# Kernel tuning notes

Measured on AMD Instinct MI355X. Metric: run time of the kernel, lower is better.

The kernel has to match this reference:

```python
import jax, jax.numpy as jnp
import numpy as np

L = 6          # num_layers
B = 2          # batch
F = 16         # num_frames
T = 64         # num_tokens per frame
S = F * T      # seq len = 1024
E = 768        # embed_dim
H = 12         # num_heads
DK = 64        # d_k
DV = 64        # d_v
DFF = 3072     # d_ff
EPS = 1e-5


def setup_inputs() -> dict:
    key = jax.random.key(0)
    ks = jax.random.split(key, 14)
    std = 0.02
    return {
        "x": jax.random.normal(ks[0], (B, S, E), jnp.float32),
        "t_pos": jax.random.normal(ks[1], (1, F, E), jnp.float32) * std,
        "s_pos": jax.random.normal(ks[2], (1, T, E), jnp.float32) * std,
        "Wq": jax.random.normal(ks[3], (L, E, H * DK), jnp.float32) * std,
        "Wk": jax.random.normal(ks[4], (L, E, H * DK), jnp.float32) * std,
        "Wv": jax.random.normal(ks[5], (L, E, H * DV), jnp.float32) * std,
        "Wo": jax.random.normal(ks[6], (L, H * DV, E), jnp.float32) * std,
        "ln1_g": jnp.ones((L, E), jnp.float32),
        "ln1_b": jnp.zeros((L, E), jnp.float32),
        "W1": jax.random.normal(ks[7], (L, E, DFF), jnp.float32) * std,
        "W2": jax.random.normal(ks[8], (L, DFF, E), jnp.float32) * std,
        "ln2_g": jnp.ones((L, E), jnp.float32),
        "ln2_b": jnp.zeros((L, E), jnp.float32),
    }


def _ln(x, g, b):
    m = jnp.mean(x, axis=-1, keepdims=True)
    v = jnp.mean(jnp.square(x - m), axis=-1, keepdims=True)
    return (x - m) * jax.lax.rsqrt(v + EPS) * g + b


def reference(x, t_pos, s_pos, Wq, Wk, Wv, Wo, ln1_g, ln1_b, W1, W2, ln2_g, ln2_b):
    # positional embeddings: frame emb repeated per token, token emb tiled per frame
    t_emb = jnp.repeat(t_pos, T, axis=1)          # [1, S, E]
    s_emb = jnp.tile(s_pos, (1, F, 1))            # [1, S, E]
    x = x + t_emb + s_emb

    # combined causal + pad mask (pad: first embed channel == 0)
    causal = jnp.triu(jnp.ones((S, S), bool), 1)[None, :, :]      # [1, S, S]
    pad = (x[:, :, 0] == 0.0)[:, None, :]                          # [B, 1, S]
    mask = (causal | pad)[:, None, :, :]                           # [B, 1, S, S]

    scale = 1.0 / np.sqrt(DK).astype(np.float32)
    attns = []
    for l in range(L):
        q = (x @ Wq[l]).reshape(B, S, H, DK).transpose(0, 2, 1, 3)  # [B,H,S,DK]
        k = (x @ Wk[l]).reshape(B, S, H, DK).transpose(0, 2, 1, 3)
        v = (x @ Wv[l]).reshape(B, S, H, DV).transpose(0, 2, 1, 3)
        scores = jnp.einsum("bhqd,bhkd->bhqk", q, k) * scale
        scores = jnp.where(mask, -1e9, scores)
        attn = jax.nn.softmax(scores, axis=-1)                      # [B,H,S,S]
        ctx = jnp.einsum("bhqk,bhkd->bhqd", attn, v)
        ctx = ctx.transpose(0, 2, 1, 3).reshape(B, S, H * DV)
        x = _ln(ctx @ Wo[l] + x, ln1_g[l], ln1_b[l])
        h = jax.nn.relu(x @ W1[l]) @ W2[l]
        x = _ln(h + x, ln2_g[l], ln2_b[l])
        attns.append(attn)
    return x, jnp.stack(attns)  # [B,S,E], [L,B,H,S,S]
```

## Files before the change

kernel.cpp:

```cpp
#include <hip/hip_runtime.h>
#include <hip/hip_bf16.h>

#define LYR  6
#define BATCH 2
#define TOK  64
#define SEQ  1024
#define EMB  768
#define HEADS 12
#define HDK  64
#define DFF  3072
#define QKVN 2304

typedef __bf16 bf16_t;
typedef __bf16 bf16x8 __attribute__((ext_vector_type(8)));
typedef float  f32x4  __attribute__((ext_vector_type(4)));
typedef unsigned int u32;

#define GLDS16(g, l) __builtin_amdgcn_global_load_lds( \
    (const __attribute__((address_space(1))) u32*)(g), \
    (__attribute__((address_space(3))) u32*)(l), 16, 0, 0)

static __device__ __forceinline__ unsigned short bfbits(float f) {
    bf16_t b = (bf16_t)f; return *(unsigned short*)&b;
}
static __device__ __forceinline__ float loadf(const void* p, size_t e, int f32) {
    if (f32) return ((const float*)p)[e];
    return (float)((const bf16_t*)p)[e];
}
static __device__ __forceinline__ ushort4 load4bf(const void* p, size_t e, int f32) {
    if (f32) {
        float4 f = *(const float4*)((const float*)p + e);
        ushort4 u; u.x = bfbits(f.x); u.y = bfbits(f.y); u.z = bfbits(f.z); u.w = bfbits(f.w);
        return u;
    }
    return *(const ushort4*)((const unsigned short*)p + e);
}

__global__ __launch_bounds__(256)
void detect_k(const void* w, int* flag)
{
    __shared__ int bad;
    if (threadIdx.x == 0) bad = 0;
    __syncthreads();
    const unsigned short* p = (const unsigned short*)w;
    int local = 0;
    for (int i = threadIdx.x; i < 4096; i += 256) {
        float v = (float)(*(const bf16_t*)&p[i]);
        if (!(v < 1e3f && v > -1e3f)) local = 1;
    }
    if (local) atomicOr(&bad, 1);
    __syncthreads();
    if (threadIdx.x == 0) *flag = bad;
}

__global__ __launch_bounds__(256)
void transp_k(const void* __restrict__ src, bf16_t* __restrict__ dst,
              int K, int N, long sstride, long dstride, long drow0, long dld,
              const int* __restrict__ flagp)
{
    __shared__ unsigned short sm[64][68];
    const int f32 = *flagp;
    const int l  = blockIdx.z;
    const int n0 = blockIdx.x * 64;
    const int k0 = blockIdx.y * 64;
    const int tid = threadIdx.x;
    const int rr = tid >> 4;
    const int cc = tid & 15;

    const size_t sb = (size_t)l * sstride;
#pragma unroll
    for (int p = 0; p < 4; p++) {
        const int kr = rr + p * 16;
        ushort4 u = load4bf(src, sb + (size_t)(k0 + kr) * N + n0 + cc * 4, f32);
        *(ushort4*)&sm[kr][cc * 4] = u;
    }
    __syncthreads();
    const size_t db = (size_t)l * dstride;
#pragma unroll
    for (int p = 0; p < 4; p++) {
        const int r2 = rr + p * 16;
        ushort4 v;
        v.x = sm[cc * 4 + 0][r2];
        v.y = sm[cc * 4 + 1][r2];
        v.z = sm[cc * 4 + 2][r2];
        v.w = sm[cc * 4 + 3][r2];
        *(ushort4*)&dst[db + (size_t)(drow0 + n0 + r2) * dld + k0 + cc * 4] = v;
    }
}

__global__ __launch_bounds__(256)
void vtr_k(const bf16_t* __restrict__ QKV, bf16_t* __restrict__ VT)
{
    __shared__ unsigned short sm[64][68];
    const int z  = blockIdx.y;
    const int s0 = blockIdx.x * 64;
    const int bq = z / HEADS, h = z % HEADS;
    const int tid = threadIdx.x;
    const int rr = tid >> 4, cc = tid & 15;
    const unsigned short* src = (const unsigned short*)QKV
        + (size_t)bq * SEQ * QKVN + 2 * EMB + (size_t)h * HDK;
#pragma unroll
    for (int p = 0; p < 4; p++) {
        const int s = rr + p * 16;
        *(ushort4*)&sm[s][cc * 4] =
            *(const ushort4*)(src + (size_t)(s0 + s) * QKVN + cc * 4);
    }
    __syncthreads();
    unsigned short* dst = (unsigned short*)VT + (size_t)z * HDK * SEQ;
#pragma unroll
    for (int p = 0; p < 4; p++) {
        const int d = rr + p * 16;
        ushort4 v;
        v.x = sm[cc * 4 + 0][d];
        v.y = sm[cc * 4 + 1][d];
        v.z = sm[cc * 4 + 2][d];
        v.w = sm[cc * 4 + 3][d];
        *(ushort4*)(dst + (size_t)d * SEQ + s0 + cc * 4) = v;
    }
}

template<int EPI>
__global__ __launch_bounds__(256)
void gemm64_k(const bf16_t* __restrict__ A, long lda,
              const bf16_t* __restrict__ BT, long ldb,
              void* __restrict__ C, long ldc, int K)
{
    __shared__ __align__(16) unsigned short As[128 * 32];
    __shared__ __align__(16) unsigned short Bs[64 * 32];

    const int tid  = threadIdx.x;
    const int lane = tid & 63;
    const int wave = tid >> 6;
    const int bm = blockIdx.x * 128;
    const int bn = blockIdx.y * 64;
    const int srow = lane >> 2;
    const int scb  = (lane & 3) * 16;
    const int l15 = lane & 15, l4 = lane >> 4;

    const char* gA = (const char*)A;
    const char* gB = (const char*)BT;

    f32x4 acc[2][4];
#pragma unroll
    for (int af = 0; af < 2; af++)
#pragma unroll
        for (int bf = 0; bf < 4; bf++) acc[af][bf] = (f32x4){0.f, 0.f, 0.f, 0.f};

    for (int k0 = 0; k0 < K; k0 += 32) {
#pragma unroll
        for (int j = 0; j < 2; j++) {
            const int rb = (j * 4 + wave) * 16;
            const char* g = gA + ((size_t)(bm + rb + srow) * lda + k0) * 2 + scb;
            GLDS16(g, &As[rb * 32]);
        }
        {
            const int rb = wave * 16;
            const char* g = gB + ((size_t)(bn + rb + srow) * ldb + k0) * 2 + scb;
            GLDS16(g, &Bs[rb * 32]);
        }
        __syncthreads();

        const bf16x8 a0 = *(const bf16x8*)&As[(wave * 32 + l15) * 32 + l4 * 8];
        const bf16x8 a1 = *(const bf16x8*)&As[(wave * 32 + 16 + l15) * 32 + l4 * 8];
#pragma unroll
        for (int bf = 0; bf < 4; bf++) {
            const bf16x8 bv = *(const bf16x8*)&Bs[(bf * 16 + l15) * 32 + l4 * 8];
            acc[0][bf] = __builtin_amdgcn_mfma_f32_16x16x32_bf16(a0, bv, acc[0][bf], 0, 0, 0);
            acc[1][bf] = __builtin_amdgcn_mfma_f32_16x16x32_bf16(a1, bv, acc[1][bf], 0, 0, 0);
        }
        __syncthreads();
    }

#pragma unroll
    for (int af = 0; af < 2; af++) {
#pragma unroll
        for (int bf = 0; bf < 4; bf++) {
#pragma unroll
            for (int r = 0; r < 4; r++) {
                const int row = bm + wave * 32 + af * 16 + l4 * 4 + r;
                const int col = bn + bf * 16 + l15;
                const float v = acc[af][bf][r];
                const size_t idx = (size_t)row * ldc + col;
                if constexpr (EPI == 0) {
                    ((bf16_t*)C)[idx] = (bf16_t)v;
                } else if constexpr (EPI == 1) {
                    ((bf16_t*)C)[idx] = (bf16_t)(v > 0.f ? v : 0.f);
                } else {
                    ((float*)C)[idx] = v;
                }
            }
        }
    }
}

template<int EPI>
__global__ __launch_bounds__(256)
void gemm128_k(const bf16_t* __restrict__ A, long lda,
               const bf16_t* __restrict__ BT, long ldb,
               void* __restrict__ C, long ldc, int K)
{
    __shared__ __align__(16) unsigned short As[128 * 32];
    __shared__ __align__(16) unsigned short Bs[128 * 32];

    const int tid  = threadIdx.x;
    const int lane = tid & 63;
    const int wave = tid >> 6;
    const int bm = blockIdx.x * 128;
    const int bn = blockIdx.y * 128;
    const int srow = lane >> 2;
    const int scb  = (lane & 3) * 16;
    const int l15 = lane & 15, l4 = lane >> 4;
    const int wr = wave >> 1, wc = wave & 1;

    const char* gA = (const char*)A;
    const char* gB = (const char*)BT;

    f32x4 acc[4][4];
#pragma unroll
    for (int m = 0; m < 4; m++)
#pragma unroll
        for (int n = 0; n < 4; n++) acc[m][n] = (f32x4){0.f, 0.f, 0.f, 0.f};

    for (int k0 = 0; k0 < K; k0 += 32) {
#pragma unroll
        for (int j = 0; j < 2; j++) {
            const int rb = (j * 4 + wave) * 16;
            const char* g = gA + ((size_t)(bm + rb + srow) * lda + k0) * 2 + scb;
            GLDS16(g, &As[rb * 32]);
        }
#pragma unroll
        for (int j = 0; j < 2; j++) {
            const int rb = (j * 4 + wave) * 16;
            const char* g = gB + ((size_t)(bn + rb + srow) * ldb + k0) * 2 + scb;
            GLDS16(g, &Bs[rb * 32]);
        }
        __syncthreads();

        bf16x8 a[4], b[4];
#pragma unroll
        for (int m = 0; m < 4; m++)
            a[m] = *(const bf16x8*)&As[(wr * 64 + m * 16 + l15) * 32 + l4 * 8];
#pragma unroll
        for (int n = 0; n < 4; n++)
            b[n] = *(const bf16x8*)&Bs[(wc * 64 + n * 16 + l15) * 32 + l4 * 8];
#pragma unroll
        for (int m = 0; m < 4; m++)
#pragma unroll
            for (int n = 0; n < 4; n++)
                acc[m][n] = __builtin_amdgcn_mfma_f32_16x16x32_bf16(a[m], b[n], acc[m][n], 0, 0, 0);
        __syncthreads();
    }

#pragma unroll
    for (int m = 0; m < 4; m++) {
#pragma unroll
        for (int n = 0; n < 4; n++) {
#pragma unroll
            for (int r = 0; r < 4; r++) {
                const int row = bm + wr * 64 + m * 16 + l4 * 4 + r;
                const int col = bn + wc * 64 + n * 16 + l15;
                const float v = acc[m][n][r];
                const size_t idx = (size_t)row * ldc + col;
                if constexpr (EPI == 0) {
                    ((bf16_t*)C)[idx] = (bf16_t)v;
                } else if constexpr (EPI == 1) {
                    ((bf16_t*)C)[idx] = (bf16_t)(v > 0.f ? v : 0.f);
                } else {
                    ((float*)C)[idx] = v;
                }
            }
        }
    }
}

__global__ __launch_bounds__(256)
void posadd_k(const void* __restrict__ x, const void* __restrict__ tp,
              const void* __restrict__ sp, float* __restrict__ X,
              bf16_t* __restrict__ XB, int* __restrict__ pad,
              const int* __restrict__ flagp)
{
    const int f32 = *flagp;
    const int row = blockIdx.x;
    const int s = row % SEQ;
    const int f = s / TOK, tt = s % TOK;
    const int tid = threadIdx.x;
#pragma unroll
    for (int i = 0; i < 3; i++) {
        int e = tid + i * 256;
        float v = loadf(x, (size_t)row * EMB + e, f32)
                + loadf(tp, (size_t)f * EMB + e, f32)
                + loadf(sp, (size_t)tt * EMB + e, f32);
        X[(size_t)row * EMB + e]  = v;
        XB[(size_t)row * EMB + e] = (bf16_t)v;
        if (e == 0) pad[row] = (v == 0.0f) ? 1 : 0;
    }
}

__global__ __launch_bounds__(256)
void attn_k(const bf16_t* __restrict__ QKV, const bf16_t* __restrict__ VT,
            bf16_t* __restrict__ CTX, void* __restrict__ outp, long probs_off,
            const int* __restrict__ pad, const int* __restrict__ flagp)
{
    __shared__ __align__(16) unsigned short P[16][1032];
    __shared__ float redm[4][16];
    __shared__ float reds[4][16];

    const int f32 = *flagp;
    const int bx  = blockIdx.x;
    const int z   = blockIdx.y;
    const int bq  = z / HEADS, h = z % HEADS;
    const int tid = threadIdx.x;
    const int lane = tid & 63;
    const int w    = tid >> 6;
    const int l15  = lane & 15;
    const int l4   = lane >> 4;

    const size_t qoff = (size_t)bq * SEQ * QKVN + (size_t)h * HDK;
    const bf16_t* Qp = QKV + qoff;
    const bf16_t* Kp = QKV + qoff + EMB;
    const bf16_t* Vt = VT + (size_t)z * HDK * SEQ;
    const int row0 = bx * 16;
    const int nt   = (bx >> 2) + 1;

    bf16x8 aq0, aq1;
    {
        const bf16_t* qp = Qp + (size_t)(row0 + l15) * QKVN + l4 * 8;
        aq0 = *(const bf16x8*)qp;
        aq1 = *(const bf16x8*)(qp + 32);
    }

    f32x4 sc[16];

#pragma unroll
    for (int ct = 0; ct < 16; ct++) {
        if (ct < nt) {
            const bf16_t* kp = Kp + (size_t)(ct * 64 + w * 16 + l15) * QKVN + l4 * 8;
            const bf16x8 b0 = *(const bf16x8*)kp;
            const bf16x8 b1 = *(const bf16x8*)(kp + 32);
            f32x4 a = (f32x4){0.f, 0.f, 0.f, 0.f};
            a = __builtin_amdgcn_mfma_f32_16x16x32_bf16(aq0, b0, a, 0, 0, 0);
            a = __builtin_amdgcn_mfma_f32_16x16x32_bf16(aq1, b1, a, 0, 0, 0);
            const int col = ct * 64 + w * 16 + l15;
            const int pd  = pad[bq * SEQ + col];
#pragma unroll
            for (int r = 0; r < 4; r++) {
                float v = a[r] * 0.125f;
                if (col > row0 + l4 * 4 + r || pd) v = -1e9f;
                sc[ct][r] = v;
            }
        }
    }

    float m4[4], s4[4];
#pragma unroll
    for (int r = 0; r < 4; r++) m4[r] = -3.0e38f;
#pragma unroll
    for (int ct = 0; ct < 16; ct++)
        if (ct < nt) {
#pragma unroll
            for (int r = 0; r < 4; r++) m4[r] = fmaxf(m4[r], sc[ct][r]);
        }
#pragma unroll
    for (int r = 0; r < 4; r++) {
        m4[r] = fmaxf(m4[r], __shfl_xor(m4[r], 1, 64));
        m4[r] = fmaxf(m4[r], __shfl_xor(m4[r], 2, 64));
        m4[r] = fmaxf(m4[r], __shfl_xor(m4[r], 4, 64));
        m4[r] = fmaxf(m4[r], __shfl_xor(m4[r], 8, 64));
    }
    if (l15 == 0) {
#pragma unroll
        for (int r = 0; r < 4; r++) redm[w][l4 * 4 + r] = m4[r];
    }
    __syncthreads();
#pragma unroll
    for (int r = 0; r < 4; r++) {
        const int row = l4 * 4 + r;
        m4[r] = fmaxf(fmaxf(redm[0][row], redm[1][row]),
                      fmaxf(redm[2][row], redm[3][row]));
        s4[r] = 0.f;
    }
#pragma unroll
    for (int ct = 0; ct < 16; ct++)
        if (ct < nt) {
#pragma unroll
            for (int r = 0; r < 4; r++) {
                float e = __expf(sc[ct][r] - m4[r]);
                sc[ct][r] = e;
                s4[r] += e;
            }
        }
#pragma unroll
    for (int r = 0; r < 4; r++) {
        s4[r] += __shfl_xor(s4[r], 1, 64);
        s4[r] += __shfl_xor(s4[r], 2, 64);
        s4[r] += __shfl_xor(s4[r], 4, 64);
        s4[r] += __shfl_xor(s4[r], 8, 64);
    }
    if (l15 == 0) {
#pragma unroll
        for (int r = 0; r < 4; r++) reds[w][l4 * 4 + r] = s4[r];
    }
    __syncthreads();
    float inv[4];
#pragma unroll
    for (int r = 0; r < 4; r++) {
        const int row = l4 * 4 + r;
        inv[r] = 1.0f / (reds[0][row] + reds[1][row] + reds[2][row] + reds[3][row]);
    }

    const size_t obase = (size_t)probs_off + ((size_t)z * SEQ + row0) * SEQ;
#pragma unroll
    for (int ct = 0; ct < 16; ct++) {
        if (ct < nt) {
            const int col = ct * 64 + w * 16 + l15;
#pragma unroll
            for (int r = 0; r < 4; r++) {
                const int row = l4 * 4 + r;
                const float p  = sc[ct][r] * inv[r];
                const float p2 = __shfl_xor(p, 1, 64);
                if (!(lane & 1)) {
                    const unsigned int pk =
                        ((unsigned int)bfbits(p2) << 16) | bfbits(p);
                    *(unsigned int*)&P[row][col] = pk;
                    if (!f32)
                        *(unsigned int*)((unsigned short*)outp + obase +
                                         (size_t)row * SEQ + col) = pk;
                }
                if (f32)
                    ((float*)outp)[obase + (size_t)row * SEQ + col] = p;
            }
        }
    }
    {
        const int c0 = nt * 64;
        if (c0 < SEQ) {
            const int rr = tid >> 4, ii = tid & 15;
            if (f32) {
                float* op = (float*)outp + obase + (size_t)rr * SEQ;
                const float4 zz = {0.f, 0.f, 0.f, 0.f};
                for (int c = c0 + ii * 4; c < SEQ; c += 64) *(float4*)(op + c) = zz;
            } else {
                unsigned short* op = (unsigned short*)outp + obase + (size_t)rr * SEQ;
                const uint4 zz = {0u, 0u, 0u, 0u};
                for (int c = c0 + ii * 8; c < SEQ; c += 128) *(uint4*)(op + c) = zz;
            }
        }
    }
    __syncthreads();

    f32x4 co = (f32x4){0.f, 0.f, 0.f, 0.f};
#pragma unroll
    for (int kt = 0; kt < 16; kt++) {
        if (kt < nt) {
            const bf16x8 a0 = *(const bf16x8*)&P[l15][kt * 64 + l4 * 8];
            const bf16x8 a1 = *(const bf16x8*)&P[l15][kt * 64 + 32 + l4 * 8];
            const bf16_t* vp = Vt + (size_t)(w * 16 + l15) * SEQ + kt * 64 + l4 * 8;
            const bf16x8 b0 = *(const bf16x8*)vp;
            const bf16x8 b1 = *(const bf16x8*)(vp + 32);
            co = __builtin_amdgcn_mfma_f32_16x16x32_bf16(a0, b0, co, 0, 0, 0);
            co = __builtin_amdgcn_mfma_f32_16x16x32_bf16(a1, b1, co, 0, 0, 0);
        }
    }
    bf16_t* cp = CTX + (size_t)bq * SEQ * EMB + (size_t)h * HDK
               + (size_t)row0 * EMB + w * 16 + l15;
#pragma unroll
    for (int r = 0; r < 4; r++)
        cp[(size_t)(l4 * 4 + r) * EMB] = (bf16_t)co[r];
}

static __device__ __forceinline__ float bsum(float v, float* red)
{
#pragma unroll
    for (int off = 32; off; off >>= 1) v += __shfl_down(v, off, 64);
    const int lane = threadIdx.x & 63, w = threadIdx.x >> 6;
    __syncthreads();
    if (lane == 0) red[w] = v;
    __syncthreads();
    return red[0] + red[1] + red[2] + red[3];
}

__global__ __launch_bounds__(256)
void ln_k(const float* __restrict__ proj, float* __restrict__ X,
          bf16_t* __restrict__ XB, const void* __restrict__ g, long goff,
          const void* __restrict__ bb, long boff2, const int* __restrict__ flagp)
{
    const int f32 = *flagp;
    const int row = blockIdx.x;
    const float* p = proj + (size_t)row * EMB;
    float* x  = X  + (size_t)row * EMB;
    bf16_t* xb = XB + (size_t)row * EMB;
    const int tid = threadIdx.x;
    __shared__ float red[4];

    float v[3];
    float sum = 0.f;
#pragma unroll
    for (int i = 0; i < 3; i++) { int e = tid + i * 256; v[i] = p[e] + x[e]; sum += v[i]; }
    sum = bsum(sum, red);
    const float mean = sum * (1.0f / EMB);

    float vs = 0.f;
#pragma unroll
    for (int i = 0; i < 3; i++) { float d = v[i] - mean; vs += d * d; }
    vs = bsum(vs, red);
    const float rstd = rsqrtf(vs * (1.0f / EMB) + 1e-5f);

#pragma unroll
    for (int i = 0; i < 3; i++) {
        int e = tid + i * 256;
        float y = (v[i] - mean) * rstd * loadf(g, goff + e, f32) + loadf(bb, boff2 + e, f32);
        x[e] = y;
        xb[e] = (bf16_t)y;
    }
}

__global__ __launch_bounds__(256)
void copyout_k(const float* __restrict__ X, void* __restrict__ outp,
               const int* __restrict__ flagp)
{
    const int f32 = *flagp;
    int i = blockIdx.x * 256 + threadIdx.x;
    float v = X[i];
    if (f32) ((float*)outp)[i] = v;
    else     ((bf16_t*)outp)[i] = (bf16_t)v;
}

extern "C" void kernel_launch(void* const* d_in, const int* in_sizes, int n_in,
                              void* d_out, int out_size, void* d_ws, size_t ws_size,
                              hipStream_t stream)
{
    const void* x  = d_in[0];
    const void* tp = d_in[1];
    const void* sp = d_in[2];
    const void* Wq = d_in[3];
    const void* Wk = d_in[4];
    const void* Wv = d_in[5];
    const void* Wo = d_in[6];
    const void* g1 = d_in[7];
    const void* b1 = d_in[8];
    const void* W1 = d_in[9];
    const void* W2 = d_in[10];
    const void* g2 = d_in[11];
    const void* b2 = d_in[12];

    const size_t BS   = (size_t)BATCH * SEQ;
    const size_t BSE  = BS * EMB;
    const size_t ATT1 = (size_t)BATCH * HEADS * SEQ * SEQ;

    char* ws = (char*)d_ws;
    size_t off = 0;
    auto alloc = [&](size_t bytes) { void* p = ws + off; off += (bytes + 255) & ~255ULL; return p; };

    float*  X     = (float*)alloc(BSE * 4);
    bf16_t* XB    = (bf16_t*)alloc(BSE * 2);
    bf16_t* QKV   = (bf16_t*)alloc(BS * QKVN * 2);
    bf16_t* VT    = (bf16_t*)alloc((size_t)BATCH * HEADS * HDK * SEQ * 2);
    bf16_t* CTXB  = (bf16_t*)alloc(BSE * 2);
    bf16_t* HB    = (bf16_t*)alloc(BS * DFF * 2);
    float*  PRJ   = (float*)alloc(BSE * 4);
    bf16_t* WqkvT = (bf16_t*)alloc((size_t)LYR * QKVN * EMB * 2);
    bf16_t* WoT   = (bf16_t*)alloc((size_t)LYR * EMB * EMB * 2);
    bf16_t* W1T   = (bf16_t*)alloc((size_t)LYR * DFF * EMB * 2);
    bf16_t* W2T   = (bf16_t*)alloc((size_t)LYR * EMB * DFF * 2);
    int*    pad   = (int*)alloc(BS * 4);
    int*    flag  = (int*)alloc(256);

    detect_k<<<dim3(1), 256, 0, stream>>>(Wq, flag);

    transp_k<<<dim3(12, 12, LYR), 256, 0, stream>>>(
        Wq, WqkvT, EMB, EMB, (long)EMB * EMB, (long)QKVN * EMB, 0, EMB, flag);
    transp_k<<<dim3(12, 12, LYR), 256, 0, stream>>>(
        Wk, WqkvT, EMB, EMB, (long)EMB * EMB, (long)QKVN * EMB, EMB, EMB, flag);
    transp_k<<<dim3(12, 12, LYR), 256, 0, stream>>>(
        Wv, WqkvT, EMB, EMB, (long)EMB * EMB, (long)QKVN * EMB, 2 * EMB, EMB, flag);
    transp_k<<<dim3(12, 12, LYR), 256, 0, stream>>>(
        Wo, WoT, EMB, EMB, (long)EMB * EMB, (long)EMB * EMB, 0, EMB, flag);
    transp_k<<<dim3(DFF / 64, 12, LYR), 256, 0, stream>>>(
        W1, W1T, EMB, DFF, (long)EMB * DFF, (long)DFF * EMB, 0, EMB, flag);
    transp_k<<<dim3(12, DFF / 64, LYR), 256, 0, stream>>>(
        W2, W2T, DFF, EMB, (long)DFF * EMB, (long)EMB * DFF, 0, DFF, flag);

    posadd_k<<<dim3((int)BS), 256, 0, stream>>>(x, tp, sp, X, XB, pad, flag);

    for (int l = 0; l < LYR; l++) {
        const long probs_off = (long)(BSE + (size_t)l * ATT1);

        gemm128_k<0><<<dim3(16, QKVN / 128), 256, 0, stream>>>(
            XB, EMB, WqkvT + (size_t)l * QKVN * EMB, EMB, QKV, QKVN, EMB);

        vtr_k<<<dim3(SEQ / 64, BATCH * HEADS), 256, 0, stream>>>(QKV, VT);

        attn_k<<<dim3(SEQ / 16, BATCH * HEADS), 256, 0, stream>>>(
            QKV, VT, CTXB, d_out, probs_off, pad, flag);

        gemm64_k<2><<<dim3(16, EMB / 64), 256, 0, stream>>>(
            CTXB, EMB, WoT + (size_t)l * EMB * EMB, EMB, PRJ, EMB, EMB);
        ln_k<<<dim3((int)BS), 256, 0, stream>>>(PRJ, X, XB, g1, (long)l * EMB, b1, (long)l * EMB, flag);

        gemm128_k<1><<<dim3(16, DFF / 128), 256, 0, stream>>>(
            XB, EMB, W1T + (size_t)l * DFF * EMB, EMB, HB, DFF, EMB);
        gemm64_k<2><<<dim3(16, EMB / 64), 256, 0, stream>>>(
            HB, DFF, W2T + (size_t)l * EMB * DFF, DFF, PRJ, EMB, DFF);
        ln_k<<<dim3((int)BS), 256, 0, stream>>>(PRJ, X, XB, g2, (long)l * EMB, b2, (long)l * EMB, flag);
    }

    copyout_k<<<dim3((int)(BSE / 256)), 256, 0, stream>>>(X, d_out, flag);
}
```

Baseline: 1.910 ms.

## Double-buffer LDS in GEMM kernels and halve M tile of 64-wide GEMM

Both GEMM kernels now keep two LDS buffers, so the global-to-LDS load for the next K step is issued before the MFMAs on the current step, and one barrier per iteration is removed. The 64-column GEMM (used for the Wo and W2 projections) drops its M tile from 128 to 64 rows, which doubles the grid from 192 to 384 blocks for the 2048x768 outputs and gives better CU coverage. The trade-off is less A/B reuse per block and more LDS per block, which can lower occupancy. The single barrier per step relies on the load into the alternate buffer being complete, with no explicit wait for the async LDS load, which could be a correctness risk.

```diff
diff --git a/kernel.cpp b/kernel.cpp
--- a/kernel.cpp
+++ b/kernel.cpp
@@ -125,13 +125,13 @@
               const bf16_t* __restrict__ BT, long ldb,
               void* __restrict__ C, long ldc, int K)
 {
-    __shared__ __align__(16) unsigned short As[128 * 32];
-    __shared__ __align__(16) unsigned short Bs[64 * 32];
+    __shared__ __align__(16) unsigned short As[2][64 * 32];
+    __shared__ __align__(16) unsigned short Bs[2][64 * 32];
 
     const int tid  = threadIdx.x;
     const int lane = tid & 63;
     const int wave = tid >> 6;
-    const int bm = blockIdx.x * 128;
+    const int bm = blockIdx.x * 64;
     const int bn = blockIdx.y * 64;
     const int srow = lane >> 2;
     const int scb  = (lane & 3) * 16;
@@ -140,54 +140,50 @@
     const char* gA = (const char*)A;
     const char* gB = (const char*)BT;
 
-    f32x4 acc[2][4];
-#pragma unroll
-    for (int af = 0; af < 2; af++)
-#pragma unroll
-        for (int bf = 0; bf < 4; bf++) acc[af][bf] = (f32x4){0.f, 0.f, 0.f, 0.f};
-
-    for (int k0 = 0; k0 < K; k0 += 32) {
-#pragma unroll
-        for (int j = 0; j < 2; j++) {
-            const int rb = (j * 4 + wave) * 16;
-            const char* g = gA + ((size_t)(bm + rb + srow) * lda + k0) * 2 + scb;
-            GLDS16(g, &As[rb * 32]);
-        }
-        {
-            const int rb = wave * 16;
-            const char* g = gB + ((size_t)(bn + rb + srow) * ldb + k0) * 2 + scb;
-            GLDS16(g, &Bs[rb * 32]);
+    f32x4 acc[4];
+#pragma unroll
+    for (int t = 0; t < 4; t++) acc[t] = (f32x4){0.f, 0.f, 0.f, 0.f};
+
+    const int nst = K >> 5;
+
+    auto stage = [&](int buf, int k0) {
+        const char* ga = gA + ((size_t)(bm + wave * 16 + srow) * lda + k0) * 2 + scb;
+        GLDS16(ga, &As[buf][wave * 16 * 32]);
+        const char* gb = gB + ((size_t)(bn + wave * 16 + srow) * ldb + k0) * 2 + scb;
+        GLDS16(gb, &Bs[buf][wave * 16 * 32]);
+    };
+
+    stage(0, 0);
+    __syncthreads();
+
+    int cur = 0;
+    for (int t = 0; t < nst; t++) {
+        if (t + 1 < nst) stage(cur ^ 1, (t + 1) << 5);
+
+        const bf16x8 av = *(const bf16x8*)&As[cur][(wave * 16 + l15) * 32 + l4 * 8];
+#pragma unroll
+        for (int bf = 0; bf < 4; bf++) {
+            const bf16x8 bv = *(const bf16x8*)&Bs[cur][(bf * 16 + l15) * 32 + l4 * 8];
+            acc[bf] = __builtin_amdgcn_mfma_f32_16x16x32_bf16(av, bv, acc[bf], 0, 0, 0);
         }
         __syncthreads();
-
-        const bf16x8 a0 = *(const bf16x8*)&As[(wave * 32 + l15) * 32 + l4 * 8];
-        const bf16x8 a1 = *(const bf16x8*)&As[(wave * 32 + 16 + l15) * 32 + l4 * 8];
-#pragma unroll
-        for (int bf = 0; bf < 4; bf++) {
-            const bf16x8 bv = *(const bf16x8*)&Bs[(bf * 16 + l15) * 32 + l4 * 8];
-            acc[0][bf] = __builtin_amdgcn_mfma_f32_16x16x32_bf16(a0, bv, acc[0][bf], 0, 0, 0);
-            acc[1][bf] = __builtin_amdgcn_mfma_f32_16x16x32_bf16(a1, bv, acc[1][bf], 0, 0, 0);
-        }
-        __syncthreads();
-    }
-
-#pragma unroll
-    for (int af = 0; af < 2; af++) {
-#pragma unroll
-        for (int bf = 0; bf < 4; bf++) {
-#pragma unroll
-            for (int r = 0; r < 4; r++) {
-                const int row = bm + wave * 32 + af * 16 + l4 * 4 + r;
-                const int col = bn + bf * 16 + l15;
-                const float v = acc[af][bf][r];
-                const size_t idx = (size_t)row * ldc + col;
-                if constexpr (EPI == 0) {
-                    ((bf16_t*)C)[idx] = (bf16_t)v;
-                } else if constexpr (EPI == 1) {
-                    ((bf16_t*)C)[idx] = (bf16_t)(v > 0.f ? v : 0.f);
-                } else {
-                    ((float*)C)[idx] = v;
-                }
+        cur ^= 1;
+    }
+
+#pragma unroll
+    for (int bf = 0; bf < 4; bf++) {
+#pragma unroll
+        for (int r = 0; r < 4; r++) {
+            const int row = bm + wave * 16 + l4 * 4 + r;
+            const int col = bn + bf * 16 + l15;
+            const float v = acc[bf][r];
+            const size_t idx = (size_t)row * ldc + col;
+            if constexpr (EPI == 0) {
+                ((bf16_t*)C)[idx] = (bf16_t)v;
+            } else if constexpr (EPI == 1) {
+                ((bf16_t*)C)[idx] = (bf16_t)(v > 0.f ? v : 0.f);
+            } else {
+                ((float*)C)[idx] = v;
             }
         }
     }
@@ -199,8 +195,8 @@
                const bf16_t* __restrict__ BT, long ldb,
                void* __restrict__ C, long ldc, int K)
 {
-    __shared__ __align__(16) unsigned short As[128 * 32];
-    __shared__ __align__(16) unsigned short Bs[128 * 32];
+    __shared__ __align__(16) unsigned short As[2][128 * 32];
+    __shared__ __align__(16) unsigned short Bs[2][128 * 32];
 
     const int tid  = threadIdx.x;
     const int lane = tid & 63;
@@ -221,34 +217,44 @@
 #pragma unroll
         for (int n = 0; n < 4; n++) acc[m][n] = (f32x4){0.f, 0.f, 0.f, 0.f};
 
-    for (int k0 = 0; k0 < K; k0 += 32) {
+    const int nst = K >> 5;
+
+    auto stage = [&](int buf, int k0) {
 #pragma unroll
         for (int j = 0; j < 2; j++) {
             const int rb = (j * 4 + wave) * 16;
-            const char* g = gA + ((size_t)(bm + rb + srow) * lda + k0) * 2 + scb;
-            GLDS16(g, &As[rb * 32]);
+            const char* ga = gA + ((size_t)(bm + rb + srow) * lda + k0) * 2 + scb;
+            GLDS16(ga, &As[buf][rb * 32]);
         }
 #pragma unroll
         for (int j = 0; j < 2; j++) {
             const int rb = (j * 4 + wave) * 16;
-            const char* g = gB + ((size_t)(bn + rb + srow) * ldb + k0) * 2 + scb;
-            GLDS16(g, &Bs[rb * 32]);
-        }
-        __syncthreads();
+            const char* gb = gB + ((size_t)(bn + rb + srow) * ldb + k0) * 2 + scb;
+            GLDS16(gb, &Bs[buf][rb * 32]);
+        }
+    };
+
+    stage(0, 0);
+    __syncthreads();
+
+    int cur = 0;
+    for (int t = 0; t < nst; t++) {
+        if (t + 1 < nst) stage(cur ^ 1, (t + 1) << 5);
 
         bf16x8 a[4], b[4];
 #pragma unroll
         for (int m = 0; m < 4; m++)
-            a[m] = *(const bf16x8*)&As[(wr * 64 + m * 16 + l15) * 32 + l4 * 8];
+            a[m] = *(const bf16x8*)&As[cur][(wr * 64 + m * 16 + l15) * 32 + l4 * 8];
 #pragma unroll
         for (int n = 0; n < 4; n++)
-            b[n] = *(const bf16x8*)&Bs[(wc * 64 + n * 16 + l15) * 32 + l4 * 8];
+            b[n] = *(const bf16x8*)&Bs[cur][(wc * 64 + n * 16 + l15) * 32 + l4 * 8];
 #pragma unroll
         for (int m = 0; m < 4; m++)
 #pragma unroll
             for (int n = 0; n < 4; n++)
                 acc[m][n] = __builtin_amdgcn_mfma_f32_16x16x32_bf16(a[m], b[n], acc[m][n], 0, 0, 0);
         __syncthreads();
+        cur ^= 1;
     }
 
 #pragma unroll
@@ -593,13 +599,13 @@
         attn_k<<<dim3(SEQ / 16, BATCH * HEADS), 256, 0, stream>>>(
             QKV, VT, CTXB, d_out, probs_off, pad, flag);
 
-        gemm64_k<2><<<dim3(16, EMB / 64), 256, 0, stream>>>(
+        gemm64_k<2><<<dim3(32, EMB / 64), 256, 0, stream>>>(
             CTXB, EMB, WoT + (size_t)l * EMB * EMB, EMB, PRJ, EMB, EMB);
         ln_k<<<dim3((int)BS), 256, 0, stream>>>(PRJ, X, XB, g1, (long)l * EMB, b1, (long)l * EMB, flag);
 
         gemm128_k<1><<<dim3(16, DFF / 128), 256, 0, stream>>>(
             XB, EMB, W1T + (size_t)l * DFF * EMB, EMB, HB, DFF, EMB);
-        gemm64_k<2><<<dim3(16, EMB / 64), 256, 0, stream>>>(
+        gemm64_k<2><<<dim3(32, EMB / 64), 256, 0, stream>>>(
             HB, DFF, W2T + (size_t)l * EMB * DFF, DFF, PRJ, EMB, DFF);
         ln_k<<<dim3((int)BS), 256, 0, stream>>>(PRJ, X, XB, g2, (long)l * EMB, b2, (long)l * EMB, flag);
     }
```

Result: faster. 1.834 ms (-4.0%).
